# Kernel optimization log

Hardware: AMD Instinct MI355X
Metric: run time of the kernel (lower is better)

The kernel has to match this reference:

```python
import jax, jax.numpy as jnp
import numpy as np

B, NQ, NK, D, H, DH = 4, 2048, 2048, 512, 8, 64  # inner_dim = H*DH = 512 = query_dim


def setup_inputs() -> dict:
    key = jax.random.key(0)
    ks = jax.random.split(key, 9)
    s = 0.02
    return {
        "init_query": jax.random.normal(ks[0], (B, NQ, D), dtype=jnp.float32),
        "embedding": jax.random.normal(ks[1], (B, NK, D), dtype=jnp.float32),
        "Wq": jax.random.normal(ks[2], (D, H * DH), dtype=jnp.float32) * s,
        "Wk": jax.random.normal(ks[3], (D, H * DH), dtype=jnp.float32) * s,
        "Wv": jax.random.normal(ks[4], (D, H * DH), dtype=jnp.float32) * s,
        "W0": jax.random.normal(ks[5], (H * DH, D), dtype=jnp.float32) * s,
        "b0": jnp.zeros((D,), dtype=jnp.float32),
        "W1": jax.random.normal(ks[6], (D, D), dtype=jnp.float32) * s,
        "b1": jnp.zeros((D,), dtype=jnp.float32),
    }


def reference(init_query, embedding, Wq, Wk, Wv, W0, b0, W1, b1):
    b, nq, _ = init_query.shape
    nk = embedding.shape[1]
    # project and split heads -> [b, h, n, dh]
    q = (init_query @ Wq).reshape(b, nq, H, DH).transpose(0, 2, 1, 3)
    k = (embedding @ Wk).reshape(b, nk, H, DH).transpose(0, 2, 1, 3)
    v = (embedding @ Wv).reshape(b, nk, H, DH).transpose(0, 2, 1, 3)
    # offset attention: alpha=1 (no 1/sqrt(d) scale)
    scores = jnp.einsum("bhqd,bhkd->bhqk", q, k)
    # softmax over the QUERY axis (torch dim=1 of [B*H, Nq, Nk]), then renormalize rows
    probs = jax.nn.softmax(scores, axis=2)
    probs = probs / (1e-12 + probs.sum(axis=-1, keepdims=True))
    out = jnp.einsum("bhqk,bhkd->bhqd", probs, v)
    out = out.transpose(0, 2, 1, 3).reshape(b, nq, H * DH)  # merge heads
    out = init_query - (out @ W0 + b0)  # offset residual
    out = out @ W1 + b1  # final projection (dropout p=0 -> identity)
    return out
```

## Files before the change

kernel.cpp:

```cpp
#include <hip/hip_runtime.h>
#include <math.h>

#define BATCH 4
#define NQ 2048
#define NKEY 2048
#define DMODEL 512
#define NH 8
#define DHEAD 64
#define BH (BATCH * NH)

typedef __attribute__((ext_vector_type(8))) short short8;
typedef __attribute__((ext_vector_type(4))) float f32x4;

#define MFMA16(a, b, c) __builtin_amdgcn_mfma_f32_16x16x32_bf16((a), (b), (c), 0, 0, 0)

static __device__ __forceinline__ unsigned short f2b(float f) {
    union { float f; unsigned u; } v; v.f = f;
    unsigned r = (v.u + 0x7fffu + ((v.u >> 16) & 1u)) >> 16;
    return (unsigned short)r;
}
static __device__ __forceinline__ float b2f(unsigned short u) {
    union { unsigned u; float f; } v; v.u = ((unsigned)u) << 16;
    return v.f;
}
static __device__ __forceinline__ unsigned pkbf(float lo, float hi) {
    unsigned r;
    asm("v_cvt_pk_bf16_f32 %0, %1, %2" : "=v"(r) : "v"(lo), "v"(hi));
    return r;
}
static __device__ __forceinline__ float ex2(float x) {
    return __builtin_amdgcn_exp2f(x);
}

__launch_bounds__(256) __global__
void cast_x(const float* __restrict__ a, const float* __restrict__ b,
            unsigned short* __restrict__ da, unsigned short* __restrict__ db) {
    const float* s = blockIdx.y ? b : a;
    unsigned short* d = blockIdx.y ? db : da;
    size_t i = ((size_t)blockIdx.x * 256 + threadIdx.x) * 4;
    float4 v = *(const float4*)(s + i);
    ushort4 o;
    o.x = f2b(v.x); o.y = f2b(v.y); o.z = f2b(v.z); o.w = f2b(v.w);
    *(ushort4*)(d + i) = o;
}

__launch_bounds__(256) __global__
void trans_w(const float* __restrict__ w0, const float* __restrict__ w1,
             const float* __restrict__ w2, const float* __restrict__ w3,
             const float* __restrict__ w4, unsigned short* __restrict__ dst) {
    const float* src = (blockIdx.z == 0) ? w0 : (blockIdx.z == 1) ? w1 :
                       (blockIdx.z == 2) ? w2 : (blockIdx.z == 3) ? w3 : w4;
    unsigned short* out = dst + (size_t)blockIdx.z * DMODEL * DMODEL;
    const float sc = (blockIdx.z == 0) ? 1.44269504088896340736f : 1.0f;
    __shared__ float t[32][33];
    const int tx = threadIdx.x & 31, ty = threadIdx.x >> 5;
    const int k0 = blockIdx.x * 32, n0 = blockIdx.y * 32;
    #pragma unroll
    for (int j = 0; j < 4; ++j)
        t[ty + j * 8][tx] = src[(size_t)(k0 + ty + j * 8) * DMODEL + n0 + tx];
    __syncthreads();
    #pragma unroll
    for (int j = 0; j < 4; ++j)
        out[(size_t)(n0 + ty + j * 8) * DMODEL + k0 + tx] = f2b(t[tx][ty + j * 8] * sc);
}

__device__ __forceinline__
void gemm_core(const unsigned short* __restrict__ A0,
               const unsigned short* __restrict__ B0,
               int K, int tid, unsigned short* Al, unsigned short* Bl,
               f32x4 acc[2][4]) {
    const int w = tid >> 6, lane = tid & 63;
    const int l16 = lane & 15, q4 = lane >> 4;
    const int srow = tid >> 3;
    const int scolb = (tid & 7) * 16;
    const int skoff = (tid & 7) * 8;

    f32x4 z = {0.f, 0.f, 0.f, 0.f};
    #pragma unroll
    for (int i = 0; i < 2; ++i)
        #pragma unroll
        for (int t = 0; t < 4; ++t) acc[i][t] = z;

    short8 ast[4], bst[2];
    #pragma unroll
    for (int c = 0; c < 4; ++c)
        ast[c] = *(const short8*)(A0 + (size_t)(c * 32 + srow) * K + skoff);
    #pragma unroll
    for (int c = 0; c < 2; ++c)
        bst[c] = *(const short8*)(B0 + (size_t)(c * 32 + srow) * K + skoff);
    {
        char* AlB = (char*)Al;
        char* BlB = (char*)Bl;
        #pragma unroll
        for (int c = 0; c < 4; ++c) {
            const int row = c * 32 + srow;
            *(short8*)(AlB + row * 128 + (scolb ^ ((row & 7) << 4))) = ast[c];
        }
        #pragma unroll
        for (int c = 0; c < 2; ++c) {
            const int row = c * 32 + srow;
            *(short8*)(BlB + row * 128 + (scolb ^ ((row & 7) << 4))) = bst[c];
        }
    }
    #pragma unroll
    for (int c = 0; c < 4; ++c)
        ast[c] = *(const short8*)(A0 + (size_t)(c * 32 + srow) * K + 64 + skoff);
    #pragma unroll
    for (int c = 0; c < 2; ++c)
        bst[c] = *(const short8*)(B0 + (size_t)(c * 32 + srow) * K + 64 + skoff);
    __syncthreads();

    const int NT = K >> 6;
    for (int t = 0; t < NT; ++t) {
        char* AlB = (char*)(Al + (t & 1) * (128 * 64));
        char* BlB = (char*)(Bl + (t & 1) * (64 * 64));
        if (t + 1 < NT) {
            char* AlN = (char*)(Al + ((t + 1) & 1) * (128 * 64));
            char* BlN = (char*)(Bl + ((t + 1) & 1) * (64 * 64));
            #pragma unroll
            for (int c = 0; c < 4; ++c) {
                const int row = c * 32 + srow;
                *(short8*)(AlN + row * 128 + (scolb ^ ((row & 7) << 4))) = ast[c];
            }
            #pragma unroll
            for (int c = 0; c < 2; ++c) {
                const int row = c * 32 + srow;
                *(short8*)(BlN + row * 128 + (scolb ^ ((row & 7) << 4))) = bst[c];
            }
            if (t + 2 < NT) {
                const int kn = (t + 2) * 64;
                #pragma unroll
                for (int c = 0; c < 4; ++c)
                    ast[c] = *(const short8*)(A0 + (size_t)(c * 32 + srow) * K + kn + skoff);
                #pragma unroll
                for (int c = 0; c < 2; ++c)
                    bst[c] = *(const short8*)(B0 + (size_t)(c * 32 + srow) * K + kn + skoff);
            }
        }

        #pragma unroll
        for (int kk = 0; kk < 2; ++kk) {
            const int kb = kk * 64;
            const int rswA0 = ((w * 32 + l16) & 7) << 4;
            short8 a0 = *(const short8*)(AlB + (w * 32 + l16) * 128 + ((kb + q4 * 16) ^ rswA0));
            short8 a1 = *(const short8*)(AlB + (w * 32 + 16 + l16) * 128 + ((kb + q4 * 16) ^ rswA0));
            short8 bfr[4];
            #pragma unroll
            for (int t2 = 0; t2 < 4; ++t2) {
                const int row = t2 * 16 + l16;
                bfr[t2] = *(const short8*)(BlB + row * 128 + ((kb + q4 * 16) ^ ((row & 7) << 4)));
            }
            #pragma unroll
            for (int t2 = 0; t2 < 4; ++t2) {
                acc[0][t2] = MFMA16(a0, bfr[t2], acc[0][t2]);
                acc[1][t2] = MFMA16(a1, bfr[t2], acc[1][t2]);
            }
        }
        __syncthreads();
    }
}

__launch_bounds__(256) __global__
void gemm_qkv(const unsigned short* __restrict__ Xq,
              const unsigned short* __restrict__ Xe,
              const unsigned short* __restrict__ Wt,
              unsigned short* __restrict__ Qh,
              unsigned short* __restrict__ Kh,
              unsigned short* __restrict__ Vtb) {
    __shared__ unsigned short Al[2][128 * 64];
    __shared__ unsigned short Bl[2][64 * 64];
    const int tid = threadIdx.x;
    const int zsel = blockIdx.z;
    const int K = DMODEL;
    const unsigned short* A = (zsel == 0) ? Xq : Xe;
    const unsigned short* B0 = Wt + (size_t)zsel * DMODEL * DMODEL + (size_t)(blockIdx.y * 64) * K;
    const unsigned short* A0 = A + (size_t)(blockIdx.x * 128) * K;

    f32x4 acc[2][4];
    gemm_core(A0, B0, K, tid, &Al[0][0], &Bl[0][0], acc);

    const int w = tid >> 6, lane = tid & 63;
    const int l16 = lane & 15, q4 = lane >> 4;
    const int mBase = blockIdx.x * 128 + w * 32;
    const int n0 = blockIdx.y * 64;

    if (zsel < 2) {
        unsigned short* out = (zsel == 0) ? Qh : Kh;
        #pragma unroll
        for (int i = 0; i < 2; ++i)
            #pragma unroll
            for (int t = 0; t < 4; ++t)
                #pragma unroll
                for (int r = 0; r < 4; ++r) {
                    const int m = mBase + i * 16 + q4 * 4 + r;
                    const int n = n0 + t * 16 + l16;
                    out[(((size_t)(m >> 11) * NH + (n >> 6)) * NQ + (m & 2047)) * DHEAD + (n & 63)] = f2b(acc[i][t][r]);
                }
    } else {
        #pragma unroll
        for (int i = 0; i < 2; ++i)
            #pragma unroll
            for (int t = 0; t < 4; ++t) {
                const int m0 = mBase + i * 16 + q4 * 4;
                const int n = n0 + t * 16 + l16;
                ushort4 p;
                p.x = f2b(acc[i][t][0]); p.y = f2b(acc[i][t][1]);
                p.z = f2b(acc[i][t][2]); p.w = f2b(acc[i][t][3]);
                *(ushort4*)(Vtb + (((size_t)(m0 >> 11) * NH + (n >> 6)) * DHEAD + (n & 63)) * NKEY + (m0 & 2047)) = p;
            }
    }
}

template <int MODE>
__launch_bounds__(256) __global__
void gemm_bf16(const unsigned short* __restrict__ A,
               const unsigned short* __restrict__ Bt,
               void* __restrict__ Cout, const float* __restrict__ bias,
               const float* __restrict__ resid, int M, int N, int K) {
    __shared__ unsigned short Al[2][128 * 64];
    __shared__ unsigned short Bl[2][64 * 64];
    const int tid = threadIdx.x;
    const unsigned short* A0 = A + (size_t)(blockIdx.x * 128) * K;
    const unsigned short* B0 = Bt + (size_t)(blockIdx.y * 64) * K;

    f32x4 acc[2][4];
    gemm_core(A0, B0, K, tid, &Al[0][0], &Bl[0][0], acc);

    const int w = tid >> 6, lane = tid & 63;
    const int l16 = lane & 15, q4 = lane >> 4;
    const int mBase = blockIdx.x * 128 + w * 32;
    const int n0 = blockIdx.y * 64;

    #pragma unroll
    for (int i = 0; i < 2; ++i)
        #pragma unroll
        for (int t = 0; t < 4; ++t)
            #pragma unroll
            for (int r = 0; r < 4; ++r) {
                const int m = mBase + i * 16 + q4 * 4 + r;
                const int n = n0 + t * 16 + l16;
                float v = acc[i][t][r];
                if (MODE == 2) {
                    ((unsigned short*)Cout)[(size_t)m * N + n] = f2b(resid[(size_t)m * N + n] - (v + bias[n]));
                } else {
                    ((float*)Cout)[(size_t)m * N + n] = v + bias[n];
                }
            }
}

__launch_bounds__(512) __global__
void attn_pass1(const unsigned short* __restrict__ Qh,
                const unsigned short* __restrict__ Kh,
                float* __restrict__ colSrcp,
                unsigned short* __restrict__ cbuf) {
    __shared__ unsigned short Qt[2][128 * 64];
    const int tid = threadIdx.x;
    const int w = tid >> 6, lane = tid & 63;
    const int l16 = lane & 15, q4 = lane >> 4;
    const int bh = blockIdx.y;
    const int kcol0 = blockIdx.x * 128 + w * 16;

    short8 bk0, bk1;
    {
        const unsigned short* Krow = Kh + ((size_t)bh * NKEY + kcol0 + l16) * DHEAD;
        bk0 = *(const short8*)(Krow + q4 * 8);
        bk1 = *(const short8*)(Krow + 32 + q4 * 8);
    }
    const unsigned short* Qb = Qh + (size_t)bh * NQ * DHEAD;
    const int srow = tid >> 3;
    const int skoff = (tid & 7) * 8;
    const int ssw = ((tid & 7) * 16) ^ ((srow & 7) << 4);
    const int rsw = (l16 & 7) << 4;

    f32x4 z = {0.f, 0.f, 0.f, 0.f};
    float csum = 0.f;

    short8 qa = *(const short8*)(Qb + (size_t)srow * DHEAD + skoff);
    short8 qb = *(const short8*)(Qb + (size_t)(64 + srow) * DHEAD + skoff);
    *(short8*)((char*)Qt[0] + srow * 128 + ssw) = qa;
    *(short8*)((char*)Qt[0] + (64 + srow) * 128 + ssw) = qb;
    qa = *(const short8*)(Qb + (size_t)(128 + srow) * DHEAD + skoff);
    qb = *(const short8*)(Qb + (size_t)(192 + srow) * DHEAD + skoff);
    __syncthreads();

    for (int it = 0; it < 16; ++it) {
        const int q0 = it * 128;
        char* QtB = (char*)Qt[it & 1];
        char* QtN = (char*)Qt[(it & 1) ^ 1];

        if (it < 15) {
            *(short8*)(QtN + srow * 128 + ssw) = qa;
            *(short8*)(QtN + (64 + srow) * 128 + ssw) = qb;
            if (it < 14) {
                qa = *(const short8*)(Qb + (size_t)(q0 + 256 + srow) * DHEAD + skoff);
                qb = *(const short8*)(Qb + (size_t)(q0 + 320 + srow) * DHEAD + skoff);
            }
        }

        #pragma unroll
        for (int qi = 0; qi < 8; ++qi) {
            const int row = qi * 16 + l16;
            short8 a0 = *(const short8*)(QtB + row * 128 + ((q4 * 16) ^ rsw));
            short8 a1 = *(const short8*)(QtB + row * 128 + ((64 + q4 * 16) ^ rsw));
            __builtin_amdgcn_s_setprio(1);
            f32x4 s = MFMA16(a0, bk0, z);
            s = MFMA16(a1, bk1, s);
            __builtin_amdgcn_s_setprio(0);
            csum += ex2(s[0]) + ex2(s[1]) + ex2(s[2]) + ex2(s[3]);
        }
        __syncthreads();
    }
    csum += __shfl_xor(csum, 16, 64);
    csum += __shfl_xor(csum, 32, 64);
    if (q4 == 0) {
        const float c = 1.0f / csum;
        const int k = kcol0 + l16;
        colSrcp[(size_t)bh * NKEY + k] = c;
        const int kloc = k & 31;
        const int nl = ((kloc & 15) >> 2) * 8 + ((kloc & 16) ? 4 : 0) + (kloc & 3);
        cbuf[(size_t)bh * NKEY + (k & ~31) + nl] = f2b(c);
    }
}

__launch_bounds__(256) __global__
void scale_v(unsigned short* __restrict__ Vtb, const float* __restrict__ colSrcp) {
    const size_t t8 = ((size_t)blockIdx.x * 256 + threadIdx.x) * 8;
    const int k = (int)(t8 & (NKEY - 1));
    const int bh = (int)(t8 >> 17);
    const float* cs = colSrcp + ((size_t)bh << 11) + k;
    short8 v = *(const short8*)(Vtb + t8);
    float4 c0 = *(const float4*)cs;
    float4 c1 = *(const float4*)(cs + 4);
    short8 o;
    o[0] = (short)f2b(b2f((unsigned short)v[0]) * c0.x);
    o[1] = (short)f2b(b2f((unsigned short)v[1]) * c0.y);
    o[2] = (short)f2b(b2f((unsigned short)v[2]) * c0.z);
    o[3] = (short)f2b(b2f((unsigned short)v[3]) * c0.w);
    o[4] = (short)f2b(b2f((unsigned short)v[4]) * c1.x);
    o[5] = (short)f2b(b2f((unsigned short)v[5]) * c1.y);
    o[6] = (short)f2b(b2f((unsigned short)v[6]) * c1.z);
    o[7] = (short)f2b(b2f((unsigned short)v[7]) * c1.w);
    *(short8*)(Vtb + t8) = o;
}

__launch_bounds__(512) __global__
void attn_pass2(const unsigned short* __restrict__ Qh,
                const unsigned short* __restrict__ Kh,
                const unsigned short* __restrict__ Vt,
                const unsigned short* __restrict__ cb,
                unsigned short* __restrict__ attnb) {
    __shared__ unsigned short Kt[2][128 * 64];
    __shared__ unsigned short Vg[2][2][64 * 64];
    const int tid = threadIdx.x;
    const int w = tid >> 6, lane = tid & 63;
    const int l16 = lane & 15, q4 = lane >> 4;
    const int bh = blockIdx.y;
    const int b = bh >> 3, h = bh & 7;
    const int q0w = blockIdx.x * 128 + w * 16;

    short8 aq0, aq1;
    {
        const unsigned short* Qrow = Qh + ((size_t)bh * NQ + q0w + l16) * DHEAD;
        aq0 = *(const short8*)(Qrow + q4 * 8);
        aq1 = *(const short8*)(Qrow + 32 + q4 * 8);
    }
    const unsigned short* Kb = Kh + (size_t)bh * NKEY * DHEAD;
    const unsigned short* Vb = Vt + (size_t)bh * DHEAD * NKEY;
    const unsigned short* cbb = cb + (size_t)bh * NKEY;

    const int srow = tid >> 3;
    const int skoff = (tid & 7) * 8;
    const int ssw = ((tid & 7) * 16) ^ ((srow & 7) << 4);
    const int rsw = (l16 & 7) << 4;
    const int local32 = skoff & 31;
    const int sub64v  = (skoff & 32) * 2;
    const int voff1 = sub64v + ((local32 >> 2) & 3) * 16 + ((local32 & 16) ? 8 : 0);
    const int rssw = (srow & 7) << 4;
    const int vsw1 = ((voff1 & 0x70) ^ rssw) | (voff1 & ~0x70);
    const int vsw2 = (((voff1 + 16) & 0x70) ^ rssw) | ((voff1 + 16) & ~0x70);

    f32x4 z = {0.f, 0.f, 0.f, 0.f};
    f32x4 o[4];
    #pragma unroll
    for (int t = 0; t < 4; ++t) o[t] = z;
    f32x4 o5 = z;

    short8 kst[2], vst[2];
    kst[0] = *(const short8*)(Kb + (size_t)srow * DHEAD + skoff);
    kst[1] = *(const short8*)(Kb + (size_t)(64 + srow) * DHEAD + skoff);
    vst[0] = *(const short8*)(Vb + (size_t)srow * NKEY + skoff);
    vst[1] = *(const short8*)(Vb + (size_t)srow * NKEY + 64 + skoff);
    {
        char* K0 = (char*)&Kt[0][0];
        char* V0 = (char*)&Vg[0][0][0];
        *(short8*)(K0 + srow * 128 + ssw) = kst[0];
        *(short8*)(K0 + (64 + srow) * 128 + ssw) = kst[1];
        union { short8 s; uint4 u; } cv0, cv1;
        cv0.s = vst[0]; cv1.s = vst[1];
        *(uint2*)(V0 + srow * 128 + vsw1) = make_uint2(cv0.u.x, cv0.u.y);
        *(uint2*)(V0 + srow * 128 + vsw2) = make_uint2(cv0.u.z, cv0.u.w);
        *(uint2*)(V0 + 8192 + srow * 128 + vsw1) = make_uint2(cv1.u.x, cv1.u.y);
        *(uint2*)(V0 + 8192 + srow * 128 + vsw2) = make_uint2(cv1.u.z, cv1.u.w);
    }
    kst[0] = *(const short8*)(Kb + (size_t)(128 + srow) * DHEAD + skoff);
    kst[1] = *(const short8*)(Kb + (size_t)(192 + srow) * DHEAD + skoff);
    vst[0] = *(const short8*)(Vb + (size_t)srow * NKEY + 128 + skoff);
    vst[1] = *(const short8*)(Vb + (size_t)srow * NKEY + 192 + skoff);
    __syncthreads();

    for (int it = 0; it < 16; ++it) {
        const int kb = it * 128;
        char* KtB = (char*)&Kt[it & 1][0];
        char* VgB = (char*)&Vg[it & 1][0][0];

        if (it < 15) {
            char* KtN = (char*)&Kt[(it & 1) ^ 1][0];
            char* VgN = (char*)&Vg[(it & 1) ^ 1][0][0];
            *(short8*)(KtN + srow * 128 + ssw) = kst[0];
            *(short8*)(KtN + (64 + srow) * 128 + ssw) = kst[1];
            union { short8 s; uint4 u; } cv0, cv1;
            cv0.s = vst[0]; cv1.s = vst[1];
            *(uint2*)(VgN + srow * 128 + vsw1) = make_uint2(cv0.u.x, cv0.u.y);
            *(uint2*)(VgN + srow * 128 + vsw2) = make_uint2(cv0.u.z, cv0.u.w);
            *(uint2*)(VgN + 8192 + srow * 128 + vsw1) = make_uint2(cv1.u.x, cv1.u.y);
            *(uint2*)(VgN + 8192 + srow * 128 + vsw2) = make_uint2(cv1.u.z, cv1.u.w);
            if (it < 14) {
                const int kn = kb + 256;
                kst[0] = *(const short8*)(Kb + (size_t)(kn + srow) * DHEAD + skoff);
                kst[1] = *(const short8*)(Kb + (size_t)(kn + 64 + srow) * DHEAD + skoff);
                vst[0] = *(const short8*)(Vb + (size_t)srow * NKEY + kn + skoff);
                vst[1] = *(const short8*)(Vb + (size_t)srow * NKEY + kn + 64 + skoff);
            }
        }

        #pragma unroll
        for (int sub = 0; sub < 4; ++sub) {
            short8 bk[2][2];
            #pragma unroll
            for (int jt = 0; jt < 2; ++jt) {
                const int row = sub * 32 + jt * 16 + l16;
                bk[jt][0] = *(const short8*)(KtB + row * 128 + ((q4 * 16) ^ rsw));
                bk[jt][1] = *(const short8*)(KtB + row * 128 + ((64 + q4 * 16) ^ rsw));
            }
            short8 bv[4];
            #pragma unroll
            for (int t = 0; t < 4; ++t) {
                const char* vrow = VgB + (sub >> 1) * 8192 + (t * 16 + l16) * 128;
                bv[t] = *(const short8*)(vrow + (((sub & 1) * 64 + q4 * 16) ^ rsw));
            }
            short8 c5 = *(const short8*)(cbb + kb + sub * 32 + q4 * 8);

            unsigned ew[4];
            #pragma unroll
            for (int jt = 0; jt < 2; ++jt) {
                __builtin_amdgcn_s_setprio(1);
                f32x4 st = MFMA16(bk[jt][0], aq0, z);
                st = MFMA16(bk[jt][1], aq1, st);
                __builtin_amdgcn_s_setprio(0);
                ew[jt * 2]     = pkbf(ex2(st[0]), ex2(st[1]));
                ew[jt * 2 + 1] = pkbf(ex2(st[2]), ex2(st[3]));
            }
            union { uint4 u; short8 s; } ea;
            ea.u = make_uint4(ew[0], ew[1], ew[2], ew[3]);

            __builtin_amdgcn_s_setprio(1);
            #pragma unroll
            for (int t = 0; t < 4; ++t)
                o[t] = MFMA16(ea.s, bv[t], o[t]);
            o5 = MFMA16(ea.s, c5, o5);
            __builtin_amdgcn_s_setprio(0);
        }
        __syncthreads();
    }

    float rr[4];
    #pragma unroll
    for (int r = 0; r < 4; ++r) rr[r] = 1.0f / (1e-12f + o5[r]);
    #pragma unroll
    for (int t = 0; t < 4; ++t)
        #pragma unroll
        for (int r = 0; r < 4; ++r) {
            const int q = q0w + q4 * 4 + r;
            attnb[((size_t)b * NQ + q) * DMODEL + h * DHEAD + t * 16 + l16] =
                f2b(o[t][r] * rr[r]);
        }
}

extern "C" void kernel_launch(void* const* d_in, const int* in_sizes, int n_in,
                              void* d_out, int out_size, void* d_ws, size_t ws_size,
                              hipStream_t stream) {
    const float* init_query = (const float*)d_in[0];
    const float* embedding  = (const float*)d_in[1];
    const float* Wq = (const float*)d_in[2];
    const float* Wk = (const float*)d_in[3];
    const float* Wv = (const float*)d_in[4];
    const float* W0 = (const float*)d_in[5];
    const float* b0 = (const float*)d_in[6];
    const float* W1 = (const float*)d_in[7];
    const float* b1 = (const float*)d_in[8];
    float* out = (float*)d_out;

    const size_t ACT = (size_t)BATCH * NQ * DMODEL;
    const size_t WEL = (size_t)DMODEL * DMODEL;

    unsigned short* Xq   = (unsigned short*)d_ws;
    unsigned short* Xe   = Xq + ACT;
    unsigned short* Wt   = Xe + ACT;
    unsigned short* Qh   = Wt + 5 * WEL;
    unsigned short* Kh   = Qh + ACT;
    unsigned short* Vtb  = Kh + ACT;
    unsigned short* attnb= Vtb + ACT;
    unsigned short* ybuf = attnb + ACT;
    float* colSrcp = (float*)(ybuf + ACT);

    unsigned short* cbuf = ybuf;

    unsigned short* W0t = Wt + 3 * WEL;
    unsigned short* W1t = Wt + 4 * WEL;

    const int M = BATCH * NQ;
    dim3 blk(256);
    dim3 blk512(512);
    dim3 gGemm(M / 128, DMODEL / 64);

    cast_x<<<dim3(ACT / 1024, 2), blk, 0, stream>>>(init_query, embedding, Xq, Xe);
    trans_w<<<dim3(16, 16, 5), blk, 0, stream>>>(Wq, Wk, Wv, W0, W1, Wt);

    gemm_qkv<<<dim3(M / 128, DMODEL / 64, 3), blk, 0, stream>>>(Xq, Xe, Wt, Qh, Kh, Vtb);

    attn_pass1<<<dim3(NKEY / 128, BH), blk512, 0, stream>>>(Qh, Kh, colSrcp, cbuf);
    scale_v<<<dim3(ACT / 2048), blk, 0, stream>>>(Vtb, colSrcp);
    attn_pass2<<<dim3(NQ / 128, BH), blk512, 0, stream>>>(Qh, Kh, Vtb, cbuf, attnb);

    gemm_bf16<2><<<gGemm, blk, 0, stream>>>(attnb, W0t, ybuf, b0, init_query, M, DMODEL, DMODEL);
    gemm_bf16<3><<<gGemm, blk, 0, stream>>>(ybuf, W1t, out, b1, nullptr, M, DMODEL, DMODEL);
}
```

Baseline: 213.5 us.

## Halve attention block size and give each wave two 16-row tiles

Both attention passes move from 512-thread to 256-thread blocks, with each wave now handling 32 keys (pass1) or 32 queries (pass2) as two 16-row MFMA tiles. Each LDS fragment of Q, K and V loaded per step is reused across two MFMA tiles, which halves LDS reads per unit of compute, and each thread now stages four global loads instead of two. In exchange, register pressure goes up and there are fewer waves per block to hide latency.

New measurement: 215.4 us. About the same (+0.9%).

```diff
diff --git a/kernel.cpp b/kernel.cpp
--- a/kernel.cpp
+++ b/kernel.cpp
@@ -248,7 +248,7 @@
             }
 }
 
-__launch_bounds__(512) __global__
+__launch_bounds__(256) __global__
 void attn_pass1(const unsigned short* __restrict__ Qh,
                 const unsigned short* __restrict__ Kh,
                 float* __restrict__ colSrcp,
@@ -258,29 +258,37 @@
     const int w = tid >> 6, lane = tid & 63;
     const int l16 = lane & 15, q4 = lane >> 4;
     const int bh = blockIdx.y;
-    const int kcol0 = blockIdx.x * 128 + w * 16;
-
-    short8 bk0, bk1;
+    const int kcol0 = blockIdx.x * 128 + w * 32;
+
+    short8 bkA0, bkA1, bkB0, bkB1;
     {
-        const unsigned short* Krow = Kh + ((size_t)bh * NKEY + kcol0 + l16) * DHEAD;
-        bk0 = *(const short8*)(Krow + q4 * 8);
-        bk1 = *(const short8*)(Krow + 32 + q4 * 8);
+        const unsigned short* KrA = Kh + ((size_t)bh * NKEY + kcol0 + l16) * DHEAD;
+        bkA0 = *(const short8*)(KrA + q4 * 8);
+        bkA1 = *(const short8*)(KrA + 32 + q4 * 8);
+        const unsigned short* KrB = KrA + (size_t)16 * DHEAD;
+        bkB0 = *(const short8*)(KrB + q4 * 8);
+        bkB1 = *(const short8*)(KrB + 32 + q4 * 8);
     }
     const unsigned short* Qb = Qh + (size_t)bh * NQ * DHEAD;
-    const int srow = tid >> 3;
+    const int sr = tid >> 3;
+    const int scb = (tid & 7) * 16;
     const int skoff = (tid & 7) * 8;
-    const int ssw = ((tid & 7) * 16) ^ ((srow & 7) << 4);
+    const int ssw = scb ^ ((sr & 7) << 4);
     const int rsw = (l16 & 7) << 4;
 
     f32x4 z = {0.f, 0.f, 0.f, 0.f};
-    float csum = 0.f;
-
-    short8 qa = *(const short8*)(Qb + (size_t)srow * DHEAD + skoff);
-    short8 qb = *(const short8*)(Qb + (size_t)(64 + srow) * DHEAD + skoff);
-    *(short8*)((char*)Qt[0] + srow * 128 + ssw) = qa;
-    *(short8*)((char*)Qt[0] + (64 + srow) * 128 + ssw) = qb;
-    qa = *(const short8*)(Qb + (size_t)(128 + srow) * DHEAD + skoff);
-    qb = *(const short8*)(Qb + (size_t)(192 + srow) * DHEAD + skoff);
+    float csumA = 0.f, csumB = 0.f;
+
+    short8 qst[4];
+    #pragma unroll
+    for (int c = 0; c < 4; ++c)
+        qst[c] = *(const short8*)(Qb + (size_t)(c * 32 + sr) * DHEAD + skoff);
+    #pragma unroll
+    for (int c = 0; c < 4; ++c)
+        *(short8*)((char*)Qt[0] + (c * 32 + sr) * 128 + ssw) = qst[c];
+    #pragma unroll
+    for (int c = 0; c < 4; ++c)
+        qst[c] = *(const short8*)(Qb + (size_t)(128 + c * 32 + sr) * DHEAD + skoff);
     __syncthreads();
 
     for (int it = 0; it < 16; ++it) {
@@ -289,11 +297,13 @@
         char* QtN = (char*)Qt[(it & 1) ^ 1];
 
         if (it < 15) {
-            *(short8*)(QtN + srow * 128 + ssw) = qa;
-            *(short8*)(QtN + (64 + srow) * 128 + ssw) = qb;
+            #pragma unroll
+            for (int c = 0; c < 4; ++c)
+                *(short8*)(QtN + (c * 32 + sr) * 128 + ssw) = qst[c];
             if (it < 14) {
-                qa = *(const short8*)(Qb + (size_t)(q0 + 256 + srow) * DHEAD + skoff);
-                qb = *(const short8*)(Qb + (size_t)(q0 + 320 + srow) * DHEAD + skoff);
+                #pragma unroll
+                for (int c = 0; c < 4; ++c)
+                    qst[c] = *(const short8*)(Qb + (size_t)(q0 + 256 + c * 32 + sr) * DHEAD + skoff);
             }
         }
 
@@ -303,22 +313,30 @@
             short8 a0 = *(const short8*)(QtB + row * 128 + ((q4 * 16) ^ rsw));
             short8 a1 = *(const short8*)(QtB + row * 128 + ((64 + q4 * 16) ^ rsw));
             __builtin_amdgcn_s_setprio(1);
-            f32x4 s = MFMA16(a0, bk0, z);
-            s = MFMA16(a1, bk1, s);
+            f32x4 sA = MFMA16(a0, bkA0, z);
+            sA = MFMA16(a1, bkA1, sA);
+            f32x4 sB = MFMA16(a0, bkB0, z);
+            sB = MFMA16(a1, bkB1, sB);
             __builtin_amdgcn_s_setprio(0);
-            csum += ex2(s[0]) + ex2(s[1]) + ex2(s[2]) + ex2(s[3]);
+            csumA += ex2(sA[0]) + ex2(sA[1]) + ex2(sA[2]) + ex2(sA[3]);
+            csumB += ex2(sB[0]) + ex2(sB[1]) + ex2(sB[2]) + ex2(sB[3]);
         }
         __syncthreads();
     }
-    csum += __shfl_xor(csum, 16, 64);
-    csum += __shfl_xor(csum, 32, 64);
+    csumA += __shfl_xor(csumA, 16, 64);
+    csumA += __shfl_xor(csumA, 32, 64);
+    csumB += __shfl_xor(csumB, 16, 64);
+    csumB += __shfl_xor(csumB, 32, 64);
     if (q4 == 0) {
-        const float c = 1.0f / csum;
-        const int k = kcol0 + l16;
-        colSrcp[(size_t)bh * NKEY + k] = c;
-        const int kloc = k & 31;
-        const int nl = ((kloc & 15) >> 2) * 8 + ((kloc & 16) ? 4 : 0) + (kloc & 3);
-        cbuf[(size_t)bh * NKEY + (k & ~31) + nl] = f2b(c);
+        #pragma unroll
+        for (int g = 0; g < 2; ++g) {
+            const float c = 1.0f / (g ? csumB : csumA);
+            const int k = kcol0 + g * 16 + l16;
+            colSrcp[(size_t)bh * NKEY + k] = c;
+            const int kloc = k & 31;
+            const int nl = ((kloc & 15) >> 2) * 8 + ((kloc & 16) ? 4 : 0) + (kloc & 3);
+            cbuf[(size_t)bh * NKEY + (k & ~31) + nl] = f2b(c);
+        }
     }
 }
 
@@ -343,7 +361,7 @@
     *(short8*)(Vtb + t8) = o;
 }
 
-__launch_bounds__(512) __global__
+__launch_bounds__(256) __global__
 void attn_pass2(const unsigned short* __restrict__ Qh,
                 const unsigned short* __restrict__ Kh,
                 const unsigned short* __restrict__ Vt,
@@ -356,56 +374,71 @@
     const int l16 = lane & 15, q4 = lane >> 4;
     const int bh = blockIdx.y;
     const int b = bh >> 3, h = bh & 7;
-    const int q0w = blockIdx.x * 128 + w * 16;
-
-    short8 aq0, aq1;
+    const int q0w = blockIdx.x * 128 + w * 32;
+
+    short8 aqA0, aqA1, aqB0, aqB1;
     {
-        const unsigned short* Qrow = Qh + ((size_t)bh * NQ + q0w + l16) * DHEAD;
-        aq0 = *(const short8*)(Qrow + q4 * 8);
-        aq1 = *(const short8*)(Qrow + 32 + q4 * 8);
+        const unsigned short* QrA = Qh + ((size_t)bh * NQ + q0w + l16) * DHEAD;
+        aqA0 = *(const short8*)(QrA + q4 * 8);
+        aqA1 = *(const short8*)(QrA + 32 + q4 * 8);
+        const unsigned short* QrB = QrA + (size_t)16 * DHEAD;
+        aqB0 = *(const short8*)(QrB + q4 * 8);
+        aqB1 = *(const short8*)(QrB + 32 + q4 * 8);
     }
     const unsigned short* Kb = Kh + (size_t)bh * NKEY * DHEAD;
     const unsigned short* Vb = Vt + (size_t)bh * DHEAD * NKEY;
     const unsigned short* cbb = cb + (size_t)bh * NKEY;
 
-    const int srow = tid >> 3;
+    const int sr = tid >> 3;
+    const int scb = (tid & 7) * 16;
     const int skoff = (tid & 7) * 8;
-    const int ssw = ((tid & 7) * 16) ^ ((srow & 7) << 4);
+    const int ksw = scb ^ ((sr & 7) << 4);
     const int rsw = (l16 & 7) << 4;
     const int local32 = skoff & 31;
     const int sub64v  = (skoff & 32) * 2;
     const int voff1 = sub64v + ((local32 >> 2) & 3) * 16 + ((local32 & 16) ? 8 : 0);
-    const int rssw = (srow & 7) << 4;
+    const int rssw = (sr & 7) << 4;
     const int vsw1 = ((voff1 & 0x70) ^ rssw) | (voff1 & ~0x70);
     const int vsw2 = (((voff1 + 16) & 0x70) ^ rssw) | ((voff1 + 16) & ~0x70);
 
     f32x4 z = {0.f, 0.f, 0.f, 0.f};
-    f32x4 o[4];
-    #pragma unroll
-    for (int t = 0; t < 4; ++t) o[t] = z;
-    f32x4 o5 = z;
-
-    short8 kst[2], vst[2];
-    kst[0] = *(const short8*)(Kb + (size_t)srow * DHEAD + skoff);
-    kst[1] = *(const short8*)(Kb + (size_t)(64 + srow) * DHEAD + skoff);
-    vst[0] = *(const short8*)(Vb + (size_t)srow * NKEY + skoff);
-    vst[1] = *(const short8*)(Vb + (size_t)srow * NKEY + 64 + skoff);
+    f32x4 o[2][4];
+    #pragma unroll
+    for (int g = 0; g < 2; ++g)
+        #pragma unroll
+        for (int t = 0; t < 4; ++t) o[g][t] = z;
+    f32x4 o5[2] = {z, z};
+
+    short8 kst[4], vst[4];
+    #pragma unroll
+    for (int c = 0; c < 4; ++c)
+        kst[c] = *(const short8*)(Kb + (size_t)(c * 32 + sr) * DHEAD + skoff);
+    vst[0] = *(const short8*)(Vb + (size_t)sr * NKEY + skoff);
+    vst[1] = *(const short8*)(Vb + (size_t)sr * NKEY + 64 + skoff);
+    vst[2] = *(const short8*)(Vb + (size_t)(32 + sr) * NKEY + skoff);
+    vst[3] = *(const short8*)(Vb + (size_t)(32 + sr) * NKEY + 64 + skoff);
     {
         char* K0 = (char*)&Kt[0][0];
         char* V0 = (char*)&Vg[0][0][0];
-        *(short8*)(K0 + srow * 128 + ssw) = kst[0];
-        *(short8*)(K0 + (64 + srow) * 128 + ssw) = kst[1];
-        union { short8 s; uint4 u; } cv0, cv1;
-        cv0.s = vst[0]; cv1.s = vst[1];
-        *(uint2*)(V0 + srow * 128 + vsw1) = make_uint2(cv0.u.x, cv0.u.y);
-        *(uint2*)(V0 + srow * 128 + vsw2) = make_uint2(cv0.u.z, cv0.u.w);
-        *(uint2*)(V0 + 8192 + srow * 128 + vsw1) = make_uint2(cv1.u.x, cv1.u.y);
-        *(uint2*)(V0 + 8192 + srow * 128 + vsw2) = make_uint2(cv1.u.z, cv1.u.w);
-    }
-    kst[0] = *(const short8*)(Kb + (size_t)(128 + srow) * DHEAD + skoff);
-    kst[1] = *(const short8*)(Kb + (size_t)(192 + srow) * DHEAD + skoff);
-    vst[0] = *(const short8*)(Vb + (size_t)srow * NKEY + 128 + skoff);
-    vst[1] = *(const short8*)(Vb + (size_t)srow * NKEY + 192 + skoff);
+        #pragma unroll
+        for (int c = 0; c < 4; ++c)
+            *(short8*)(K0 + (c * 32 + sr) * 128 + ksw) = kst[c];
+        #pragma unroll
+        for (int p = 0; p < 4; ++p) {
+            union { short8 s; uint4 u; } cv; cv.s = vst[p];
+            const int row = (p >> 1) * 32 + sr;
+            char* gbase = V0 + (p & 1) * 8192 + row * 128;
+            *(uint2*)(gbase + vsw1) = make_uint2(cv.u.x, cv.u.y);
+            *(uint2*)(gbase + vsw2) = make_uint2(cv.u.z, cv.u.w);
+        }
+    }
+    #pragma unroll
+    for (int c = 0; c < 4; ++c)
+        kst[c] = *(const short8*)(Kb + (size_t)(128 + c * 32 + sr) * DHEAD + skoff);
+    vst[0] = *(const short8*)(Vb + (size_t)sr * NKEY + 128 + skoff);
+    vst[1] = *(const short8*)(Vb + (size_t)sr * NKEY + 192 + skoff);
+    vst[2] = *(const short8*)(Vb + (size_t)(32 + sr) * NKEY + 128 + skoff);
+    vst[3] = *(const short8*)(Vb + (size_t)(32 + sr) * NKEY + 192 + skoff);
     __syncthreads();
 
     for (int it = 0; it < 16; ++it) {
@@ -416,20 +449,26 @@
         if (it < 15) {
             char* KtN = (char*)&Kt[(it & 1) ^ 1][0];
             char* VgN = (char*)&Vg[(it & 1) ^ 1][0][0];
-            *(short8*)(KtN + srow * 128 + ssw) = kst[0];
-            *(short8*)(KtN + (64 + srow) * 128 + ssw) = kst[1];
-            union { short8 s; uint4 u; } cv0, cv1;
-            cv0.s = vst[0]; cv1.s = vst[1];
-            *(uint2*)(VgN + srow * 128 + vsw1) = make_uint2(cv0.u.x, cv0.u.y);
-            *(uint2*)(VgN + srow * 128 + vsw2) = make_uint2(cv0.u.z, cv0.u.w);
-            *(uint2*)(VgN + 8192 + srow * 128 + vsw1) = make_uint2(cv1.u.x, cv1.u.y);
-            *(uint2*)(VgN + 8192 + srow * 128 + vsw2) = make_uint2(cv1.u.z, cv1.u.w);
+            #pragma unroll
+            for (int c = 0; c < 4; ++c)
+                *(short8*)(KtN + (c * 32 + sr) * 128 + ksw) = kst[c];
+            #pragma unroll
+            for (int p = 0; p < 4; ++p) {
+                union { short8 s; uint4 u; } cv; cv.s = vst[p];
+                const int row = (p >> 1) * 32 + sr;
+                char* gbase = VgN + (p & 1) * 8192 + row * 128;
+                *(uint2*)(gbase + vsw1) = make_uint2(cv.u.x, cv.u.y);
+                *(uint2*)(gbase + vsw2) = make_uint2(cv.u.z, cv.u.w);
+            }
             if (it < 14) {
                 const int kn = kb + 256;
-                kst[0] = *(const short8*)(Kb + (size_t)(kn + srow) * DHEAD + skoff);
-                kst[1] = *(const short8*)(Kb + (size_t)(kn + 64 + srow) * DHEAD + skoff);
-                vst[0] = *(const short8*)(Vb + (size_t)srow * NKEY + kn + skoff);
-                vst[1] = *(const short8*)(Vb + (size_t)srow * NKEY + kn + 64 + skoff);
+                #pragma unroll
+                for (int c = 0; c < 4; ++c)
+                    kst[c] = *(const short8*)(Kb + (size_t)(kn + c * 32 + sr) * DHEAD + skoff);
+                vst[0] = *(const short8*)(Vb + (size_t)sr * NKEY + kn + skoff);
+                vst[1] = *(const short8*)(Vb + (size_t)sr * NKEY + kn + 64 + skoff);
+                vst[2] = *(const short8*)(Vb + (size_t)(32 + sr) * NKEY + kn + skoff);
+                vst[3] = *(const short8*)(Vb + (size_t)(32 + sr) * NKEY + kn + 64 + skoff);
             }
         }
 
@@ -450,40 +489,52 @@
             }
             short8 c5 = *(const short8*)(cbb + kb + sub * 32 + q4 * 8);
 
-            unsigned ew[4];
+            unsigned ewA[4], ewB[4];
             #pragma unroll
             for (int jt = 0; jt < 2; ++jt) {
                 __builtin_amdgcn_s_setprio(1);
-                f32x4 st = MFMA16(bk[jt][0], aq0, z);
-                st = MFMA16(bk[jt][1], aq1, st);
+                f32x4 stA = MFMA16(bk[jt][0], aqA0, z);
+                stA = MFMA16(bk[jt][1], aqA1, stA);
+                f32x4 stB = MFMA16(bk[jt][0], aqB0, z);
+                stB = MFMA16(bk[jt][1], aqB1, stB);
                 __builtin_amdgcn_s_setprio(0);
-                ew[jt * 2]     = pkbf(ex2(st[0]), ex2(st[1]));
-                ew[jt * 2 + 1] = pkbf(ex2(st[2]), ex2(st[3]));
-            }
-            union { uint4 u; short8 s; } ea;
-            ea.u = make_uint4(ew[0], ew[1], ew[2], ew[3]);
+                ewA[jt * 2]     = pkbf(ex2(stA[0]), ex2(stA[1]));
+                ewA[jt * 2 + 1] = pkbf(ex2(stA[2]), ex2(stA[3]));
+                ewB[jt * 2]     = pkbf(ex2(stB[0]), ex2(stB[1]));
+                ewB[jt * 2 + 1] = pkbf(ex2(stB[2]), ex2(stB[3]));
+            }
+            union { uint4 u; short8 s; } eaA, eaB;
+            eaA.u = make_uint4(ewA[0], ewA[1], ewA[2], ewA[3]);
+            eaB.u = make_uint4(ewB[0], ewB[1], ewB[2], ewB[3]);
 
             __builtin_amdgcn_s_setprio(1);
             #pragma unroll
             for (int t = 0; t < 4; ++t)
-                o[t] = MFMA16(ea.s, bv[t], o[t]);
-            o5 = MFMA16(ea.s, c5, o5);
+                o[0][t] = MFMA16(eaA.s, bv[t], o[0][t]);
+            o5[0] = MFMA16(eaA.s, c5, o5[0]);
+            #pragma unroll
+            for (int t = 0; t < 4; ++t)
+                o[1][t] = MFMA16(eaB.s, bv[t], o[1][t]);
+            o5[1] = MFMA16(eaB.s, c5, o5[1]);
             __builtin_amdgcn_s_setprio(0);
         }
         __syncthreads();
     }
 
-    float rr[4];
-    #pragma unroll
-    for (int r = 0; r < 4; ++r) rr[r] = 1.0f / (1e-12f + o5[r]);
-    #pragma unroll
-    for (int t = 0; t < 4; ++t)
-        #pragma unroll
-        for (int r = 0; r < 4; ++r) {
-            const int q = q0w + q4 * 4 + r;
-            attnb[((size_t)b * NQ + q) * DMODEL + h * DHEAD + t * 16 + l16] =
-                f2b(o[t][r] * rr[r]);
-        }
+    #pragma unroll
+    for (int g = 0; g < 2; ++g) {
+        float rr[4];
+        #pragma unroll
+        for (int r = 0; r < 4; ++r) rr[r] = 1.0f / (1e-12f + o5[g][r]);
+        #pragma unroll
+        for (int t = 0; t < 4; ++t)
+            #pragma unroll
+            for (int r = 0; r < 4; ++r) {
+                const int q = q0w + g * 16 + q4 * 4 + r;
+                attnb[((size_t)b * NQ + q) * DMODEL + h * DHEAD + t * 16 + l16] =
+                    f2b(o[g][t][r] * rr[r]);
+            }
+    }
 }
 
 extern "C" void kernel_launch(void* const* d_in, const int* in_sizes, int n_in,
@@ -520,7 +571,6 @@
 
     const int M = BATCH * NQ;
     dim3 blk(256);
-    dim3 blk512(512);
     dim3 gGemm(M / 128, DMODEL / 64);
 
     cast_x<<<dim3(ACT / 1024, 2), blk, 0, stream>>>(init_query, embedding, Xq, Xe);
@@ -528,9 +578,9 @@
 
     gemm_qkv<<<dim3(M / 128, DMODEL / 64, 3), blk, 0, stream>>>(Xq, Xe, Wt, Qh, Kh, Vtb);
 
-    attn_pass1<<<dim3(NKEY / 128, BH), blk512, 0, stream>>>(Qh, Kh, colSrcp, cbuf);
+    attn_pass1<<<dim3(NKEY / 128, BH), blk, 0, stream>>>(Qh, Kh, colSrcp, cbuf);
     scale_v<<<dim3(ACT / 2048), blk, 0, stream>>>(Vtb, colSrcp);
-    attn_pass2<<<dim3(NQ / 128, BH), blk512, 0, stream>>>(Qh, Kh, Vtb, cbuf, attnb);
+    attn_pass2<<<dim3(NQ / 128, BH), blk, 0, stream>>>(Qh, Kh, Vtb, cbuf, attnb);
 
     gemm_bf16<2><<<gGemm, blk, 0, stream>>>(attnb, W0t, ybuf, b0, init_query, M, DMODEL, DMODEL);
     gemm_bf16<3><<<gGemm, blk, 0, stream>>>(ybuf, W1t, out, b1, nullptr, M, DMODEL, DMODEL);
```

## Stage GEMM tiles with direct global-to-LDS loads instead of register staging

Applied to the files above, without the earlier changes.

Replaces the register-staged double-buffered tile loads in the shared GEMM core with global_load_lds 16-byte transfers that write straight into LDS. The XOR swizzle is moved onto the global source address so the LDS layout seen by the MFMA reads stays the same. The next-next tile is issued after the barrier into the buffer just consumed. This is meant to save VGPRs and the separate ds_write instructions. It relies on the barrier waiting for the async loads, which may add stall time.

Measured after the change: 215.0 us. No clear change (+0.7%).

```diff
diff --git a/kernel.cpp b/kernel.cpp
--- a/kernel.cpp
+++ b/kernel.cpp
@@ -30,6 +30,11 @@
 }
 static __device__ __forceinline__ float ex2(float x) {
     return __builtin_amdgcn_exp2f(x);
+}
+static __device__ __forceinline__ void gload16(const void* g, void* l) {
+    __builtin_amdgcn_global_load_lds(
+        (const __attribute__((address_space(1))) void*)g,
+        (__attribute__((address_space(3))) void*)l, 16, 0, 0);
 }
 
 __launch_bounds__(256) __global__
@@ -71,9 +76,8 @@
                f32x4 acc[2][4]) {
     const int w = tid >> 6, lane = tid & 63;
     const int l16 = lane & 15, q4 = lane >> 4;
-    const int srow = tid >> 3;
-    const int scolb = (tid & 7) * 16;
-    const int skoff = (tid & 7) * 8;
+    const int lrow = lane >> 3;
+    const int lsrc = ((lane & 7) ^ lrow) * 8;
 
     f32x4 z = {0.f, 0.f, 0.f, 0.f};
     #pragma unroll
@@ -81,62 +85,33 @@
         #pragma unroll
         for (int t = 0; t < 4; ++t) acc[i][t] = z;
 
-    short8 ast[4], bst[2];
-    #pragma unroll
-    for (int c = 0; c < 4; ++c)
-        ast[c] = *(const short8*)(A0 + (size_t)(c * 32 + srow) * K + skoff);
-    #pragma unroll
-    for (int c = 0; c < 2; ++c)
-        bst[c] = *(const short8*)(B0 + (size_t)(c * 32 + srow) * K + skoff);
-    {
-        char* AlB = (char*)Al;
-        char* BlB = (char*)Bl;
-        #pragma unroll
-        for (int c = 0; c < 4; ++c) {
-            const int row = c * 32 + srow;
-            *(short8*)(AlB + row * 128 + (scolb ^ ((row & 7) << 4))) = ast[c];
-        }
-        #pragma unroll
-        for (int c = 0; c < 2; ++c) {
-            const int row = c * 32 + srow;
-            *(short8*)(BlB + row * 128 + (scolb ^ ((row & 7) << 4))) = bst[c];
-        }
-    }
-    #pragma unroll
-    for (int c = 0; c < 4; ++c)
-        ast[c] = *(const short8*)(A0 + (size_t)(c * 32 + srow) * K + 64 + skoff);
-    #pragma unroll
-    for (int c = 0; c < 2; ++c)
-        bst[c] = *(const short8*)(B0 + (size_t)(c * 32 + srow) * K + 64 + skoff);
+    auto issueA = [&](unsigned short* Ad, int kbase) {
+        #pragma unroll
+        for (int i = 0; i < 4; ++i) {
+            const int cg = w * 4 + i;
+            gload16(A0 + (size_t)(cg * 8 + lrow) * K + kbase + lsrc,
+                    (char*)Ad + cg * 1024);
+        }
+    };
+    auto issueB = [&](unsigned short* Bd, int kbase) {
+        #pragma unroll
+        for (int j = 0; j < 2; ++j) {
+            const int cg = w * 2 + j;
+            gload16(B0 + (size_t)(cg * 8 + lrow) * K + kbase + lsrc,
+                    (char*)Bd + cg * 1024);
+        }
+    };
+
+    issueA(Al, 0);
+    issueB(Bl, 0);
     __syncthreads();
+    issueA(Al + 128 * 64, 64);
+    issueB(Bl + 64 * 64, 64);
 
     const int NT = K >> 6;
     for (int t = 0; t < NT; ++t) {
         char* AlB = (char*)(Al + (t & 1) * (128 * 64));
         char* BlB = (char*)(Bl + (t & 1) * (64 * 64));
-        if (t + 1 < NT) {
-            char* AlN = (char*)(Al + ((t + 1) & 1) * (128 * 64));
-            char* BlN = (char*)(Bl + ((t + 1) & 1) * (64 * 64));
-            #pragma unroll
-            for (int c = 0; c < 4; ++c) {
-                const int row = c * 32 + srow;
-                *(short8*)(AlN + row * 128 + (scolb ^ ((row & 7) << 4))) = ast[c];
-            }
-            #pragma unroll
-            for (int c = 0; c < 2; ++c) {
-                const int row = c * 32 + srow;
-                *(short8*)(BlN + row * 128 + (scolb ^ ((row & 7) << 4))) = bst[c];
-            }
-            if (t + 2 < NT) {
-                const int kn = (t + 2) * 64;
-                #pragma unroll
-                for (int c = 0; c < 4; ++c)
-                    ast[c] = *(const short8*)(A0 + (size_t)(c * 32 + srow) * K + kn + skoff);
-                #pragma unroll
-                for (int c = 0; c < 2; ++c)
-                    bst[c] = *(const short8*)(B0 + (size_t)(c * 32 + srow) * K + kn + skoff);
-            }
-        }
 
         #pragma unroll
         for (int kk = 0; kk < 2; ++kk) {
@@ -157,6 +132,10 @@
             }
         }
         __syncthreads();
+        if (t + 2 < NT) {
+            issueA(Al + (t & 1) * (128 * 64), (t + 2) * 64);
+            issueB(Bl + (t & 1) * (64 * 64), (t + 2) * 64);
+        }
     }
 }
 
```
